# Kernel optimization log

Hardware: AMD Instinct MI355X
Metric: run time of the kernel (lower is better)

The kernel has to match this reference:

```python
import jax, jax.numpy as jnp
import numpy as np

B, H, W, C = 8, 128, 128, 128
SCALE = C ** -0.5
EPS = 1e-6  # flax LayerNorm default


def layer_norm(x, scale, bias):
    m = jnp.mean(x, axis=-1, keepdims=True)
    v = jnp.var(x, axis=-1, keepdims=True)
    return (x - m) * jax.lax.rsqrt(v + EPS) * scale + bias


def setup_inputs() -> dict:
    key = jax.random.key(0)
    ks = jax.random.split(key, 12)
    std = 0.02
    return {
        "x_l": jax.random.normal(ks[0], (B, H, W, C), jnp.float32),
        "x_r": jax.random.normal(ks[1], (B, H, W, C), jnp.float32),
        "ln_l_scale": jnp.ones((C,), jnp.float32),
        "ln_l_bias": jnp.zeros((C,), jnp.float32),
        "ln_r_scale": jnp.ones((C,), jnp.float32),
        "ln_r_bias": jnp.zeros((C,), jnp.float32),
        "w_ql": jax.random.normal(ks[2], (C, C), jnp.float32) * std,
        "b_ql": jnp.zeros((C,), jnp.float32),
        "w_qr": jax.random.normal(ks[3], (C, C), jnp.float32) * std,
        "b_qr": jnp.zeros((C,), jnp.float32),
        "w_vl": jax.random.normal(ks[4], (C, C), jnp.float32) * std,
        "b_vl": jnp.zeros((C,), jnp.float32),
        "w_vr": jax.random.normal(ks[5], (C, C), jnp.float32) * std,
        "b_vr": jnp.zeros((C,), jnp.float32),
        "beta": jax.random.normal(ks[6], (1, 1, 1, C), jnp.float32) * std,
        "gamma": jax.random.normal(ks[7], (1, 1, 1, C), jnp.float32) * std,
    }


def reference(x_l, x_r, ln_l_scale, ln_l_bias, ln_r_scale, ln_r_bias,
              w_ql, b_ql, w_qr, b_qr, w_vl, b_vl, w_vr, b_vr, beta, gamma):
    # Q projections of layer-normed inputs  [B,H,W,C]
    q_l = layer_norm(x_l, ln_l_scale, ln_l_bias) @ w_ql + b_ql
    q_r = layer_norm(x_r, ln_r_scale, ln_r_bias) @ w_qr + b_qr
    # V projections of raw inputs
    v_l = x_l @ w_vl + b_vl
    v_r = x_r @ w_vr + b_vr
    # shared cross-view score matrix over the width axis: [B,H,W_l,W_r]
    attention = jnp.einsum('bhic,bhjc->bhij', q_l, q_r) * SCALE
    # dual softmax: rows (axis=-1) and transposed columns
    f_r2l = jnp.einsum('bhij,bhjc->bhic', jax.nn.softmax(attention, axis=-1), v_r) * beta
    f_l2r = jnp.einsum('bhji,bhjc->bhic',
                       jax.nn.softmax(attention, axis=-2), v_l) * gamma
    return (x_l + f_r2l, x_r + f_l2r)
```

## Files before the change

kernel.cpp:

```cpp
#include <hip/hip_runtime.h>


typedef __attribute__((ext_vector_type(8))) __bf16 bf16x8;
typedef __attribute__((ext_vector_type(4))) __bf16 bf16x4;
typedef __attribute__((ext_vector_type(4))) float f4;

#define MFMA(A, B, C) __builtin_amdgcn_mfma_f32_16x16x32_bf16((A), (B), (C), 0, 0, 0)
#define SCALE_QK 0.08838834764831845f

static __device__ __forceinline__ int eoff(int n, int k) {
  return (n << 8) + ((((k >> 3) ^ (n & 7)) << 4) | ((k & 7) << 1));
}

__global__ void prep_w(const float* __restrict__ w0, const float* __restrict__ w1,
                       const float* __restrict__ w2, const float* __restrict__ w3,
                       __bf16* __restrict__ out) {
  int m = blockIdx.y;
  const float* src = (m == 0) ? w0 : (m == 1) ? w1 : (m == 2) ? w2 : w3;
  int t = blockIdx.x * 256 + threadIdx.x;
  int k = t >> 7, n = t & 127;
  out[m * 16384 + n * 128 + k] = (__bf16)src[k * 128 + n];
}

static __device__ __forceinline__ void stage_w(char* slot, const __bf16* __restrict__ wTm,
                                               int tid) {
#pragma unroll
  for (int it = 0; it < 8; ++it) {
    int idx = it * 256 + tid;
    int n = idx >> 4, seg = idx & 15;
    uint4 v = *(const uint4*)(wTm + n * 128 + seg * 8);
    *(uint4*)(slot + (n << 8) + ((seg ^ (n & 7)) << 4)) = v;
  }
}

static __device__ __forceinline__ void load_side(
    const float* __restrict__ xp, size_t base, const float* __restrict__ g,
    const float* __restrict__ b, char* xs, char* ls, int w, int lane, int l16, int quad,
    bf16x8* xF, bf16x8* lF) {
  int half = lane >> 5;
  int c4 = (lane & 31) << 2;
  float4 gv = *(const float4*)(g + c4);
  float4 bv = *(const float4*)(b + c4);
#pragma unroll
  for (int i = 0; i < 16; ++i) {
    int row = w * 32 + i * 2 + half;
    float4 xv = *(const float4*)(xp + base + row * 128 + c4);
    float s = xv.x + xv.y + xv.z + xv.w;
    float s2 = xv.x * xv.x + xv.y * xv.y + xv.z * xv.z + xv.w * xv.w;
#pragma unroll
    for (int d = 1; d < 32; d <<= 1) {
      s += __shfl_xor(s, d);
      s2 += __shfl_xor(s2, d);
    }
    float mean = s * 0.0078125f;
    float var = s2 * 0.0078125f - mean * mean;
    float rstd = rsqrtf(var + 1e-6f);
    bf16x4 xu, lu;
    xu[0] = (__bf16)xv.x; xu[1] = (__bf16)xv.y; xu[2] = (__bf16)xv.z; xu[3] = (__bf16)xv.w;
    lu[0] = (__bf16)((xv.x - mean) * rstd * gv.x + bv.x);
    lu[1] = (__bf16)((xv.y - mean) * rstd * gv.y + bv.y);
    lu[2] = (__bf16)((xv.z - mean) * rstd * gv.z + bv.z);
    lu[3] = (__bf16)((xv.w - mean) * rstd * gv.w + bv.w);
    int off = eoff(row, c4);
    *(bf16x4*)(xs + off) = xu;
    *(bf16x4*)(ls + off) = lu;
  }
  __syncthreads();
#pragma unroll
  for (int mt = 0; mt < 2; ++mt)
#pragma unroll
    for (int ks = 0; ks < 4; ++ks) {
      int row = w * 32 + mt * 16 + l16, k = ks * 32 + quad * 8;
      xF[mt * 4 + ks] = *(const bf16x8*)(xs + eoff(row, k));
      lF[mt * 4 + ks] = *(const bf16x8*)(ls + eoff(row, k));
    }
  __syncthreads();
}

template <int TRANSPOSED>
static __device__ __forceinline__ void proj(const bf16x8* aF, const char* wslot, char* dst,
                                            const float* __restrict__ bias, float scale,
                                            int w, int l16, int quad) {
#pragma unroll
  for (int nt = 0; nt < 8; ++nt) {
    f4 a0 = {0.f, 0.f, 0.f, 0.f}, a1 = {0.f, 0.f, 0.f, 0.f};
#pragma unroll
    for (int ks = 0; ks < 4; ++ks) {
      bf16x8 bf = *(const bf16x8*)(wslot + eoff(nt * 16 + l16, ks * 32 + quad * 8));
      a0 = MFMA(aF[ks], bf, a0);
      a1 = MFMA(aF[4 + ks], bf, a1);
    }
    float bs = bias[nt * 16 + l16];
    if (TRANSPOSED) {
      int c = nt * 16 + l16;
#pragma unroll
      for (int mt = 0; mt < 2; ++mt) {
        f4 a = mt ? a1 : a0;
        bf16x4 v;
#pragma unroll
        for (int r = 0; r < 4; ++r) v[r] = (__bf16)((a[r] + bs) * scale);
        *(bf16x4*)(dst + eoff(c, w * 32 + mt * 16 + quad * 4)) = v;
      }
    } else {
#pragma unroll
      for (int mt = 0; mt < 2; ++mt) {
        f4 a = mt ? a1 : a0;
#pragma unroll
        for (int r = 0; r < 4; ++r) {
          int i = w * 32 + mt * 16 + quad * 4 + r;
          *(__bf16*)(dst + eoff(i, nt * 16 + l16)) = (__bf16)((a[r] + bs) * scale);
        }
      }
    }
  }
}

static __device__ __forceinline__ void pv(const bf16x8* pF, const char* vslot, char* fdst,
                                          int w, int l16, int quad) {
#pragma unroll
  for (int nt = 0; nt < 8; ++nt) {
    f4 a0 = {0.f, 0.f, 0.f, 0.f}, a1 = {0.f, 0.f, 0.f, 0.f};
#pragma unroll
    for (int ks = 0; ks < 4; ++ks) {
      bf16x8 bf = *(const bf16x8*)(vslot + eoff(nt * 16 + l16, ks * 32 + quad * 8));
      a0 = MFMA(pF[ks], bf, a0);
      a1 = MFMA(pF[4 + ks], bf, a1);
    }
#pragma unroll
    for (int mt = 0; mt < 2; ++mt) {
      f4 a = mt ? a1 : a0;
#pragma unroll
      for (int r = 0; r < 4; ++r) {
        int i = w * 32 + mt * 16 + quad * 4 + r;
        *(__bf16*)(fdst + eoff(i, nt * 16 + l16)) = (__bf16)a[r];
      }
    }
  }
}

static __device__ __forceinline__ void epilogue(const float* __restrict__ xp, size_t base,
                                                const float* __restrict__ scl,
                                                const char* fsrc, float* __restrict__ outp,
                                                int tid) {
#pragma unroll
  for (int it = 0; it < 16; ++it) {
    int idx = it * 256 + tid;
    int row = idx >> 5, cb = (idx & 31) << 2;
    float4 xv = *(const float4*)(xp + base + row * 128 + cb);
    float4 sv = *(const float4*)(scl + cb);
    bf16x4 fu = *(const bf16x4*)(fsrc + eoff(row, cb));
    float4 ov;
    ov.x = xv.x + sv.x * (float)fu[0];
    ov.y = xv.y + sv.y * (float)fu[1];
    ov.z = xv.z + sv.z * (float)fu[2];
    ov.w = xv.w + sv.w * (float)fu[3];
    *(float4*)(outp + base + row * 128 + cb) = ov;
  }
}

__global__ __launch_bounds__(256, 2) void scam_fused(
    const float* __restrict__ xl, const float* __restrict__ xr,
    const float* __restrict__ gl, const float* __restrict__ bl,
    const float* __restrict__ gr, const float* __restrict__ br,
    const __bf16* __restrict__ wT,
    const float* __restrict__ bql, const float* __restrict__ bqr,
    const float* __restrict__ bvl, const float* __restrict__ bvr,
    const float* __restrict__ beta, const float* __restrict__ gamma,
    float* __restrict__ out0, float* __restrict__ out1) {
  __shared__ char smem[65536];
  char* S1 = smem;
  char* S2 = smem + 32768;
  int tid = threadIdx.x;
  int lane = tid & 63, w = tid >> 6;
  int quad = lane >> 4, l16 = lane & 15;
  size_t base = (size_t)blockIdx.x << 14;

  bf16x8 xlF[8], llF[8], xrF[8], lrF[8];
  load_side(xl, base, gl, bl, S1, S2, w, lane, l16, quad, xlF, llF);
  load_side(xr, base, gr, br, S1, S2, w, lane, l16, quad, xrF, lrF);

  stage_w(S1, wT, tid);
  __syncthreads();
  proj<0>(llF, S1, S2, bql, SCALE_QK, w, l16, quad);
  __syncthreads();
  bf16x8 qlF[8];
#pragma unroll
  for (int mt = 0; mt < 2; ++mt)
#pragma unroll
    for (int ks = 0; ks < 4; ++ks)
      qlF[mt * 4 + ks] =
          *(const bf16x8*)(S2 + eoff(w * 32 + mt * 16 + l16, ks * 32 + quad * 8));
  __syncthreads();

  stage_w(S1, wT + 16384, tid);
  __syncthreads();
  proj<0>(lrF, S1, S2, bqr, 1.0f, w, l16, quad);
  __syncthreads();

  f4 sacc[2][8];
  const f4 fzero = {0.f, 0.f, 0.f, 0.f};
#pragma unroll
  for (int mt = 0; mt < 2; ++mt)
#pragma unroll
    for (int nt = 0; nt < 8; ++nt) sacc[mt][nt] = fzero;
#pragma unroll
  for (int nt = 0; nt < 8; ++nt)
#pragma unroll
    for (int ks = 0; ks < 4; ++ks) {
      bf16x8 bf = *(const bf16x8*)(S2 + eoff(nt * 16 + l16, ks * 32 + quad * 8));
      sacc[0][nt] = MFMA(qlF[ks], bf, sacc[0][nt]);
      sacc[1][nt] = MFMA(qlF[4 + ks], bf, sacc[1][nt]);
    }

  float rm[2][4], rinv[2][4];
#pragma unroll
  for (int mt = 0; mt < 2; ++mt)
#pragma unroll
    for (int r = 0; r < 4; ++r) {
      float m = -1e30f;
#pragma unroll
      for (int nt = 0; nt < 8; ++nt) m = fmaxf(m, sacc[mt][nt][r]);
#pragma unroll
      for (int d = 1; d < 16; d <<= 1) m = fmaxf(m, __shfl_xor(m, d));
      float s = 0.f;
#pragma unroll
      for (int nt = 0; nt < 8; ++nt) s += __expf(sacc[mt][nt][r] - m);
#pragma unroll
      for (int d = 1; d < 16; d <<= 1) s += __shfl_xor(s, d);
      rm[mt][r] = m;
      rinv[mt][r] = 1.f / s;
    }
  float* colred = (float*)S1;
  float cm[8], cinv[8];
#pragma unroll
  for (int nt = 0; nt < 8; ++nt) {
    float m = -1e30f;
#pragma unroll
    for (int mt = 0; mt < 2; ++mt)
#pragma unroll
      for (int r = 0; r < 4; ++r) m = fmaxf(m, sacc[mt][nt][r]);
    m = fmaxf(m, __shfl_xor(m, 16));
    m = fmaxf(m, __shfl_xor(m, 32));
    cm[nt] = m;
  }
  __syncthreads();
  if (quad == 0) {
#pragma unroll
    for (int nt = 0; nt < 8; ++nt) colred[w * 128 + nt * 16 + l16] = cm[nt];
  }
  __syncthreads();
#pragma unroll
  for (int nt = 0; nt < 8; ++nt) {
    float m = cm[nt];
#pragma unroll
    for (int ww = 0; ww < 4; ++ww) m = fmaxf(m, colred[ww * 128 + nt * 16 + l16]);
    cm[nt] = m;
  }
  __syncthreads();
#pragma unroll
  for (int nt = 0; nt < 8; ++nt) {
    float s = 0.f;
#pragma unroll
    for (int mt = 0; mt < 2; ++mt)
#pragma unroll
      for (int r = 0; r < 4; ++r) s += __expf(sacc[mt][nt][r] - cm[nt]);
    s += __shfl_xor(s, 16);
    s += __shfl_xor(s, 32);
    cinv[nt] = s;
  }
  if (quad == 0) {
#pragma unroll
    for (int nt = 0; nt < 8; ++nt) colred[w * 128 + nt * 16 + l16] = cinv[nt];
  }
  __syncthreads();
#pragma unroll
  for (int nt = 0; nt < 8; ++nt) {
    float s = 0.f;
#pragma unroll
    for (int ww = 0; ww < 4; ++ww) s += colred[ww * 128 + nt * 16 + l16];
    cinv[nt] = 1.f / s;
  }
  __syncthreads();

#pragma unroll
  for (int mt = 0; mt < 2; ++mt)
#pragma unroll
    for (int nt = 0; nt < 8; ++nt) {
      bf16x4 pc;
#pragma unroll
      for (int r = 0; r < 4; ++r) {
        float sv = sacc[mt][nt][r];
        int i = w * 32 + mt * 16 + quad * 4 + r;
        *(__bf16*)(S1 + eoff(i, nt * 16 + l16)) =
            (__bf16)(__expf(sv - rm[mt][r]) * rinv[mt][r]);
        pc[r] = (__bf16)(__expf(sv - cm[nt]) * cinv[nt]);
      }
      *(bf16x4*)(S2 + eoff(nt * 16 + l16, w * 32 + mt * 16 + quad * 4)) = pc;
    }
  __syncthreads();
  bf16x8 prF[8], pcF[8];
#pragma unroll
  for (int mt = 0; mt < 2; ++mt)
#pragma unroll
    for (int ks = 0; ks < 4; ++ks) {
      int row = w * 32 + mt * 16 + l16, k = ks * 32 + quad * 8;
      prF[mt * 4 + ks] = *(const bf16x8*)(S1 + eoff(row, k));
      pcF[mt * 4 + ks] = *(const bf16x8*)(S2 + eoff(row, k));
    }
  __syncthreads();

  stage_w(S1, wT + 3 * 16384, tid);
  __syncthreads();
  proj<1>(xrF, S1, S2, bvr, 1.0f, w, l16, quad);
  __syncthreads();
  pv(prF, S2, S1, w, l16, quad);
  __syncthreads();
  epilogue(xl, base, beta, S1, out0, tid);
  __syncthreads();

  stage_w(S1, wT + 2 * 16384, tid);
  __syncthreads();
  proj<1>(xlF, S1, S2, bvl, 1.0f, w, l16, quad);
  __syncthreads();
  pv(pcF, S2, S1, w, l16, quad);
  __syncthreads();
  epilogue(xr, base, gamma, S1, out1, tid);
}

extern "C" void kernel_launch(void* const* d_in, const int* in_sizes, int n_in,
                              void* d_out, int out_size, void* d_ws, size_t ws_size,
                              hipStream_t stream) {
  const float* xl = (const float*)d_in[0];
  const float* xr = (const float*)d_in[1];
  const float* gl = (const float*)d_in[2];
  const float* bl = (const float*)d_in[3];
  const float* gr = (const float*)d_in[4];
  const float* br = (const float*)d_in[5];
  const float* wql = (const float*)d_in[6];
  const float* bql = (const float*)d_in[7];
  const float* wqr = (const float*)d_in[8];
  const float* bqr = (const float*)d_in[9];
  const float* wvl = (const float*)d_in[10];
  const float* bvl = (const float*)d_in[11];
  const float* wvr = (const float*)d_in[12];
  const float* bvr = (const float*)d_in[13];
  const float* beta = (const float*)d_in[14];
  const float* gamma = (const float*)d_in[15];

  __bf16* wT = (__bf16*)d_ws;
  float* out0 = (float*)d_out;
  float* out1 = out0 + (size_t)8 * 128 * 128 * 128;

  prep_w<<<dim3(64, 4), 256, 0, stream>>>(wql, wqr, wvl, wvr, wT);
  scam_fused<<<1024, 256, 0, stream>>>(xl, xr, gl, bl, gr, br, wT, bql, bqr, bvl, bvr,
                                       beta, gamma, out0, out1);
}
```

Before: 416.7 us.

## Halve LDS footprint and read weights/inputs directly from global to raise occupancy

Shrinks shared memory from 64KB to about 34KB and raises the launch bound from 2 to 4 blocks per CU. Weight tiles are no longer staged through LDS; MFMA B fragments are read straight from global (L2-cached) memory. Input and layernorm fragments are built directly from global loads rather than via an LDS round trip. The PV result is fused with the residual epilogue and written with scalar global stores. In exchange, x is reloaded from global several times, and the output stores become strided scalar writes instead of coalesced float4.

```diff
diff --git a/kernel.cpp b/kernel.cpp
--- a/kernel.cpp
+++ b/kernel.cpp
@@ -22,143 +22,164 @@
   out[m * 16384 + n * 128 + k] = (__bf16)src[k * 128 + n];
 }
 
-static __device__ __forceinline__ void stage_w(char* slot, const __bf16* __restrict__ wTm,
-                                               int tid) {
-#pragma unroll
-  for (int it = 0; it < 8; ++it) {
-    int idx = it * 256 + tid;
-    int n = idx >> 4, seg = idx & 15;
-    uint4 v = *(const uint4*)(wTm + n * 128 + seg * 8);
-    *(uint4*)(slot + (n << 8) + ((seg ^ (n & 7)) << 4)) = v;
-  }
-}
-
-static __device__ __forceinline__ void load_side(
-    const float* __restrict__ xp, size_t base, const float* __restrict__ g,
-    const float* __restrict__ b, char* xs, char* ls, int w, int lane, int l16, int quad,
-    bf16x8* xF, bf16x8* lF) {
-  int half = lane >> 5;
-  int c4 = (lane & 31) << 2;
-  float4 gv = *(const float4*)(g + c4);
-  float4 bv = *(const float4*)(b + c4);
-#pragma unroll
-  for (int i = 0; i < 16; ++i) {
-    int row = w * 32 + i * 2 + half;
-    float4 xv = *(const float4*)(xp + base + row * 128 + c4);
-    float s = xv.x + xv.y + xv.z + xv.w;
-    float s2 = xv.x * xv.x + xv.y * xv.y + xv.z * xv.z + xv.w * xv.w;
-#pragma unroll
-    for (int d = 1; d < 32; d <<= 1) {
-      s += __shfl_xor(s, d);
-      s2 += __shfl_xor(s2, d);
-    }
+static __device__ __forceinline__ void build_x_frags(const float* __restrict__ xp,
+                                                     size_t base, int w, int l16,
+                                                     int quad, bf16x8* F) {
+#pragma unroll
+  for (int mt = 0; mt < 2; ++mt) {
+    const float* rp = xp + base + (size_t)(w * 32 + mt * 16 + l16) * 128;
+#pragma unroll
+    for (int ks = 0; ks < 4; ++ks) {
+      int k0 = ks * 32 + quad * 8;
+      float4 p0 = *(const float4*)(rp + k0);
+      float4 p1 = *(const float4*)(rp + k0 + 4);
+      bf16x8 f;
+      f[0] = (__bf16)p0.x; f[1] = (__bf16)p0.y; f[2] = (__bf16)p0.z; f[3] = (__bf16)p0.w;
+      f[4] = (__bf16)p1.x; f[5] = (__bf16)p1.y; f[6] = (__bf16)p1.z; f[7] = (__bf16)p1.w;
+      F[mt * 4 + ks] = f;
+    }
+  }
+}
+
+static __device__ __forceinline__ void build_ln_frags(const float* __restrict__ xp,
+                                                      size_t base,
+                                                      const float* __restrict__ g,
+                                                      const float* __restrict__ b,
+                                                      int w, int l16, int quad,
+                                                      bf16x8* F) {
+#pragma unroll
+  for (int mt = 0; mt < 2; ++mt) {
+    const float* rp = xp + base + (size_t)(w * 32 + mt * 16 + l16) * 128;
+    float4 v[8];
+#pragma unroll
+    for (int ks = 0; ks < 4; ++ks) {
+      int k0 = ks * 32 + quad * 8;
+      v[ks * 2] = *(const float4*)(rp + k0);
+      v[ks * 2 + 1] = *(const float4*)(rp + k0 + 4);
+    }
+    float s = 0.f, s2 = 0.f;
+#pragma unroll
+    for (int t = 0; t < 8; ++t) {
+      s += v[t].x + v[t].y + v[t].z + v[t].w;
+      s2 += v[t].x * v[t].x + v[t].y * v[t].y + v[t].z * v[t].z + v[t].w * v[t].w;
+    }
+    s += __shfl_xor(s, 16); s2 += __shfl_xor(s2, 16);
+    s += __shfl_xor(s, 32); s2 += __shfl_xor(s2, 32);
     float mean = s * 0.0078125f;
     float var = s2 * 0.0078125f - mean * mean;
     float rstd = rsqrtf(var + 1e-6f);
-    bf16x4 xu, lu;
-    xu[0] = (__bf16)xv.x; xu[1] = (__bf16)xv.y; xu[2] = (__bf16)xv.z; xu[3] = (__bf16)xv.w;
-    lu[0] = (__bf16)((xv.x - mean) * rstd * gv.x + bv.x);
-    lu[1] = (__bf16)((xv.y - mean) * rstd * gv.y + bv.y);
-    lu[2] = (__bf16)((xv.z - mean) * rstd * gv.z + bv.z);
-    lu[3] = (__bf16)((xv.w - mean) * rstd * gv.w + bv.w);
-    int off = eoff(row, c4);
-    *(bf16x4*)(xs + off) = xu;
-    *(bf16x4*)(ls + off) = lu;
-  }
-  __syncthreads();
-#pragma unroll
-  for (int mt = 0; mt < 2; ++mt)
-#pragma unroll
-    for (int ks = 0; ks < 4; ++ks) {
-      int row = w * 32 + mt * 16 + l16, k = ks * 32 + quad * 8;
-      xF[mt * 4 + ks] = *(const bf16x8*)(xs + eoff(row, k));
-      lF[mt * 4 + ks] = *(const bf16x8*)(ls + eoff(row, k));
-    }
-  __syncthreads();
-}
-
-template <int TRANSPOSED>
-static __device__ __forceinline__ void proj(const bf16x8* aF, const char* wslot, char* dst,
-                                            const float* __restrict__ bias, float scale,
-                                            int w, int l16, int quad) {
-#pragma unroll
-  for (int nt = 0; nt < 8; ++nt) {
+#pragma unroll
+    for (int ks = 0; ks < 4; ++ks) {
+      int k0 = ks * 32 + quad * 8;
+      float4 g0 = *(const float4*)(g + k0), g1 = *(const float4*)(g + k0 + 4);
+      float4 b0 = *(const float4*)(b + k0), b1 = *(const float4*)(b + k0 + 4);
+      float4 p0 = v[ks * 2], p1 = v[ks * 2 + 1];
+      bf16x8 f;
+      f[0] = (__bf16)((p0.x - mean) * rstd * g0.x + b0.x);
+      f[1] = (__bf16)((p0.y - mean) * rstd * g0.y + b0.y);
+      f[2] = (__bf16)((p0.z - mean) * rstd * g0.z + b0.z);
+      f[3] = (__bf16)((p0.w - mean) * rstd * g0.w + b0.w);
+      f[4] = (__bf16)((p1.x - mean) * rstd * g1.x + b1.x);
+      f[5] = (__bf16)((p1.y - mean) * rstd * g1.y + b1.y);
+      f[6] = (__bf16)((p1.z - mean) * rstd * g1.z + b1.z);
+      f[7] = (__bf16)((p1.w - mean) * rstd * g1.w + b1.w);
+      F[mt * 4 + ks] = f;
+    }
+  }
+}
+
+static __device__ __forceinline__ void proj_q(const bf16x8* aF,
+                                              const __bf16* __restrict__ wTm, char* slot,
+                                              const float* __restrict__ bias, float scale,
+                                              int w, int l16, int quad) {
+#pragma unroll
+  for (int nt = 0; nt < 8; ++nt) {
+    int n = nt * 16 + l16;
     f4 a0 = {0.f, 0.f, 0.f, 0.f}, a1 = {0.f, 0.f, 0.f, 0.f};
 #pragma unroll
     for (int ks = 0; ks < 4; ++ks) {
-      bf16x8 bf = *(const bf16x8*)(wslot + eoff(nt * 16 + l16, ks * 32 + quad * 8));
+      bf16x8 bf = *(const bf16x8*)(wTm + n * 128 + ks * 32 + quad * 8);
       a0 = MFMA(aF[ks], bf, a0);
       a1 = MFMA(aF[4 + ks], bf, a1);
     }
-    float bs = bias[nt * 16 + l16];
-    if (TRANSPOSED) {
-      int c = nt * 16 + l16;
-#pragma unroll
-      for (int mt = 0; mt < 2; ++mt) {
-        f4 a = mt ? a1 : a0;
-        bf16x4 v;
-#pragma unroll
-        for (int r = 0; r < 4; ++r) v[r] = (__bf16)((a[r] + bs) * scale);
-        *(bf16x4*)(dst + eoff(c, w * 32 + mt * 16 + quad * 4)) = v;
+    float bs = bias[n];
+#pragma unroll
+    for (int mt = 0; mt < 2; ++mt) {
+      f4 a = mt ? a1 : a0;
+#pragma unroll
+      for (int r = 0; r < 4; ++r) {
+        int i = w * 32 + mt * 16 + quad * 4 + r;
+        *(__bf16*)(slot + eoff(i, n)) = (__bf16)((a[r] + bs) * scale);
       }
-    } else {
-#pragma unroll
-      for (int mt = 0; mt < 2; ++mt) {
-        f4 a = mt ? a1 : a0;
-#pragma unroll
-        for (int r = 0; r < 4; ++r) {
-          int i = w * 32 + mt * 16 + quad * 4 + r;
-          *(__bf16*)(dst + eoff(i, nt * 16 + l16)) = (__bf16)((a[r] + bs) * scale);
-        }
-      }
-    }
-  }
-}
-
-static __device__ __forceinline__ void pv(const bf16x8* pF, const char* vslot, char* fdst,
-                                          int w, int l16, int quad) {
-#pragma unroll
-  for (int nt = 0; nt < 8; ++nt) {
+    }
+  }
+}
+
+static __device__ __forceinline__ void proj_vT(const bf16x8* aF,
+                                               const __bf16* __restrict__ wTm, char* slot,
+                                               const float* __restrict__ bias, int w,
+                                               int l16, int quad) {
+#pragma unroll
+  for (int nt = 0; nt < 8; ++nt) {
+    int n = nt * 16 + l16;
     f4 a0 = {0.f, 0.f, 0.f, 0.f}, a1 = {0.f, 0.f, 0.f, 0.f};
 #pragma unroll
     for (int ks = 0; ks < 4; ++ks) {
-      bf16x8 bf = *(const bf16x8*)(vslot + eoff(nt * 16 + l16, ks * 32 + quad * 8));
+      bf16x8 bf = *(const bf16x8*)(wTm + n * 128 + ks * 32 + quad * 8);
+      a0 = MFMA(aF[ks], bf, a0);
+      a1 = MFMA(aF[4 + ks], bf, a1);
+    }
+    float bs = bias[n];
+#pragma unroll
+    for (int mt = 0; mt < 2; ++mt) {
+      f4 a = mt ? a1 : a0;
+      bf16x4 vv;
+#pragma unroll
+      for (int r = 0; r < 4; ++r) vv[r] = (__bf16)(a[r] + bs);
+      *(bf16x4*)(slot + eoff(n, w * 32 + mt * 16 + quad * 4)) = vv;
+    }
+  }
+}
+
+static __device__ __forceinline__ void pv_epi(const bf16x8* pF, const char* slot,
+                                              const float* __restrict__ xp, size_t base,
+                                              const float* __restrict__ scl,
+                                              float* __restrict__ outp, int w, int l16,
+                                              int quad) {
+#pragma unroll
+  for (int nt = 0; nt < 8; ++nt) {
+    int c = nt * 16 + l16;
+    f4 a0 = {0.f, 0.f, 0.f, 0.f}, a1 = {0.f, 0.f, 0.f, 0.f};
+#pragma unroll
+    for (int ks = 0; ks < 4; ++ks) {
+      bf16x8 bf = *(const bf16x8*)(slot + eoff(c, ks * 32 + quad * 8));
       a0 = MFMA(pF[ks], bf, a0);
       a1 = MFMA(pF[4 + ks], bf, a1);
     }
+    float sc = scl[c];
 #pragma unroll
     for (int mt = 0; mt < 2; ++mt) {
       f4 a = mt ? a1 : a0;
 #pragma unroll
       for (int r = 0; r < 4; ++r) {
-        int i = w * 32 + mt * 16 + quad * 4 + r;
-        *(__bf16*)(fdst + eoff(i, nt * 16 + l16)) = (__bf16)a[r];
+        size_t off = base + (size_t)(w * 32 + mt * 16 + quad * 4 + r) * 128 + c;
+        outp[off] = xp[off] + sc * a[r];
       }
     }
   }
 }
 
-static __device__ __forceinline__ void epilogue(const float* __restrict__ xp, size_t base,
-                                                const float* __restrict__ scl,
-                                                const char* fsrc, float* __restrict__ outp,
-                                                int tid) {
-#pragma unroll
-  for (int it = 0; it < 16; ++it) {
-    int idx = it * 256 + tid;
-    int row = idx >> 5, cb = (idx & 31) << 2;
-    float4 xv = *(const float4*)(xp + base + row * 128 + cb);
-    float4 sv = *(const float4*)(scl + cb);
-    bf16x4 fu = *(const bf16x4*)(fsrc + eoff(row, cb));
-    float4 ov;
-    ov.x = xv.x + sv.x * (float)fu[0];
-    ov.y = xv.y + sv.y * (float)fu[1];
-    ov.z = xv.z + sv.z * (float)fu[2];
-    ov.w = xv.w + sv.w * (float)fu[3];
-    *(float4*)(outp + base + row * 128 + cb) = ov;
-  }
-}
-
-__global__ __launch_bounds__(256, 2) void scam_fused(
+static __device__ __forceinline__ void read_afrags(const char* slot, int w, int l16,
+                                                   int quad, bf16x8* F) {
+#pragma unroll
+  for (int mt = 0; mt < 2; ++mt)
+#pragma unroll
+    for (int ks = 0; ks < 4; ++ks)
+      F[mt * 4 + ks] =
+          *(const bf16x8*)(slot + eoff(w * 32 + mt * 16 + l16, ks * 32 + quad * 8));
+}
+
+__global__ __launch_bounds__(256, 4) void scam_fused(
     const float* __restrict__ xl, const float* __restrict__ xr,
     const float* __restrict__ gl, const float* __restrict__ bl,
     const float* __restrict__ gr, const float* __restrict__ br,
@@ -167,34 +188,28 @@
     const float* __restrict__ bvl, const float* __restrict__ bvr,
     const float* __restrict__ beta, const float* __restrict__ gamma,
     float* __restrict__ out0, float* __restrict__ out1) {
-  __shared__ char smem[65536];
-  char* S1 = smem;
-  char* S2 = smem + 32768;
+  __shared__ char slot[32768];
+  __shared__ float colred[512];
   int tid = threadIdx.x;
   int lane = tid & 63, w = tid >> 6;
   int quad = lane >> 4, l16 = lane & 15;
   size_t base = (size_t)blockIdx.x << 14;
 
-  bf16x8 xlF[8], llF[8], xrF[8], lrF[8];
-  load_side(xl, base, gl, bl, S1, S2, w, lane, l16, quad, xlF, llF);
-  load_side(xr, base, gr, br, S1, S2, w, lane, l16, quad, xrF, lrF);
-
-  stage_w(S1, wT, tid);
-  __syncthreads();
-  proj<0>(llF, S1, S2, bql, SCALE_QK, w, l16, quad);
+  {
+    bf16x8 lF[8];
+    build_ln_frags(xl, base, gl, bl, w, l16, quad, lF);
+    proj_q(lF, wT, slot, bql, SCALE_QK, w, l16, quad);
+  }
   __syncthreads();
   bf16x8 qlF[8];
-#pragma unroll
-  for (int mt = 0; mt < 2; ++mt)
-#pragma unroll
-    for (int ks = 0; ks < 4; ++ks)
-      qlF[mt * 4 + ks] =
-          *(const bf16x8*)(S2 + eoff(w * 32 + mt * 16 + l16, ks * 32 + quad * 8));
-  __syncthreads();
-
-  stage_w(S1, wT + 16384, tid);
-  __syncthreads();
-  proj<0>(lrF, S1, S2, bqr, 1.0f, w, l16, quad);
+  read_afrags(slot, w, l16, quad, qlF);
+  __syncthreads();
+
+  {
+    bf16x8 lF[8];
+    build_ln_frags(xr, base, gr, br, w, l16, quad, lF);
+    proj_q(lF, wT + 16384, slot, bqr, 1.0f, w, l16, quad);
+  }
   __syncthreads();
 
   f4 sacc[2][8];
@@ -207,7 +222,7 @@
   for (int nt = 0; nt < 8; ++nt)
 #pragma unroll
     for (int ks = 0; ks < 4; ++ks) {
-      bf16x8 bf = *(const bf16x8*)(S2 + eoff(nt * 16 + l16, ks * 32 + quad * 8));
+      bf16x8 bf = *(const bf16x8*)(slot + eoff(nt * 16 + l16, ks * 32 + quad * 8));
       sacc[0][nt] = MFMA(qlF[ks], bf, sacc[0][nt]);
       sacc[1][nt] = MFMA(qlF[4 + ks], bf, sacc[1][nt]);
     }
@@ -230,7 +245,6 @@
       rm[mt][r] = m;
       rinv[mt][r] = 1.f / s;
     }
-  float* colred = (float*)S1;
   float cm[8], cinv[8];
 #pragma unroll
   for (int nt = 0; nt < 8; ++nt) {
@@ -256,7 +270,16 @@
     for (int ww = 0; ww < 4; ++ww) m = fmaxf(m, colred[ww * 128 + nt * 16 + l16]);
     cm[nt] = m;
   }
-  __syncthreads();
+#pragma unroll
+  for (int mt = 0; mt < 2; ++mt)
+#pragma unroll
+    for (int nt = 0; nt < 8; ++nt)
+#pragma unroll
+      for (int r = 0; r < 4; ++r) {
+        int i = w * 32 + mt * 16 + quad * 4 + r;
+        *(__bf16*)(slot + eoff(i, nt * 16 + l16)) =
+            (__bf16)(__expf(sacc[mt][nt][r] - rm[mt][r]) * rinv[mt][r]);
+      }
 #pragma unroll
   for (int nt = 0; nt < 8; ++nt) {
     float s = 0.f;
@@ -268,6 +291,7 @@
     s += __shfl_xor(s, 32);
     cinv[nt] = s;
   }
+  __syncthreads();
   if (quad == 0) {
 #pragma unroll
     for (int nt = 0; nt < 8; ++nt) colred[w * 128 + nt * 16 + l16] = cinv[nt];
@@ -280,51 +304,40 @@
     for (int ww = 0; ww < 4; ++ww) s += colred[ww * 128 + nt * 16 + l16];
     cinv[nt] = 1.f / s;
   }
-  __syncthreads();
-
+  bf16x8 prF[8];
+  read_afrags(slot, w, l16, quad, prF);
+  __syncthreads();
 #pragma unroll
   for (int mt = 0; mt < 2; ++mt)
 #pragma unroll
     for (int nt = 0; nt < 8; ++nt) {
       bf16x4 pc;
 #pragma unroll
-      for (int r = 0; r < 4; ++r) {
-        float sv = sacc[mt][nt][r];
-        int i = w * 32 + mt * 16 + quad * 4 + r;
-        *(__bf16*)(S1 + eoff(i, nt * 16 + l16)) =
-            (__bf16)(__expf(sv - rm[mt][r]) * rinv[mt][r]);
-        pc[r] = (__bf16)(__expf(sv - cm[nt]) * cinv[nt]);
-      }
-      *(bf16x4*)(S2 + eoff(nt * 16 + l16, w * 32 + mt * 16 + quad * 4)) = pc;
-    }
-  __syncthreads();
-  bf16x8 prF[8], pcF[8];
-#pragma unroll
-  for (int mt = 0; mt < 2; ++mt)
-#pragma unroll
-    for (int ks = 0; ks < 4; ++ks) {
-      int row = w * 32 + mt * 16 + l16, k = ks * 32 + quad * 8;
-      prF[mt * 4 + ks] = *(const bf16x8*)(S1 + eoff(row, k));
-      pcF[mt * 4 + ks] = *(const bf16x8*)(S2 + eoff(row, k));
-    }
-  __syncthreads();
-
-  stage_w(S1, wT + 3 * 16384, tid);
-  __syncthreads();
-  proj<1>(xrF, S1, S2, bvr, 1.0f, w, l16, quad);
-  __syncthreads();
-  pv(prF, S2, S1, w, l16, quad);
-  __syncthreads();
-  epilogue(xl, base, beta, S1, out0, tid);
-  __syncthreads();
-
-  stage_w(S1, wT + 2 * 16384, tid);
-  __syncthreads();
-  proj<1>(xlF, S1, S2, bvl, 1.0f, w, l16, quad);
-  __syncthreads();
-  pv(pcF, S2, S1, w, l16, quad);
-  __syncthreads();
-  epilogue(xr, base, gamma, S1, out1, tid);
+      for (int r = 0; r < 4; ++r)
+        pc[r] = (__bf16)(__expf(sacc[mt][nt][r] - cm[nt]) * cinv[nt]);
+      *(bf16x4*)(slot + eoff(nt * 16 + l16, w * 32 + mt * 16 + quad * 4)) = pc;
+    }
+  __syncthreads();
+  bf16x8 pcF[8];
+  read_afrags(slot, w, l16, quad, pcF);
+  __syncthreads();
+
+  {
+    bf16x8 xF[8];
+    build_x_frags(xr, base, w, l16, quad, xF);
+    proj_vT(xF, wT + 3 * 16384, slot, bvr, w, l16, quad);
+  }
+  __syncthreads();
+  pv_epi(prF, slot, xl, base, beta, out0, w, l16, quad);
+  __syncthreads();
+
+  {
+    bf16x8 xF[8];
+    build_x_frags(xl, base, w, l16, quad, xF);
+    proj_vT(xF, wT + 2 * 16384, slot, bvl, w, l16, quad);
+  }
+  __syncthreads();
+  pv_epi(pcF, slot, xr, base, gamma, out1, w, l16, quad);
 }
 
 extern "C" void kernel_launch(void* const* d_in, const int* in_sizes, int n_in,
```

New measurement: 605.1 us. 1.45x slower.
